# Kernel tuning notes

Hardware: AMD Instinct MI355X
Metric: run time of the kernel (lower is better)

Reference implementation:

```python
import jax, jax.numpy as jnp
import numpy as np

DROP_BLOCK = 7  # matches init_kwargs drop_block


def setup_inputs() -> dict:
    key = jax.random.key(0)
    k1, k2 = jax.random.split(key)
    x = jax.random.normal(k1, (32, 512, 56, 56), dtype=jnp.float32)
    T = jax.random.randint(k2, (32, 512, 1, 1), 0, 2, dtype=jnp.int32)
    return {"x": x, "T": T}


def _local_mask(x, T):
    B, C, H, W = x.shape
    xf = x.reshape(-1, H, W)                      # [B*C, H, W]
    marked = (T.reshape(-1) > 0)                  # [B*C] bool; which channels get a cutout
    # Argmax location per channel (original uses h for both div and mod)
    idx = jnp.argmax(xf.reshape(xf.shape[0], -1), axis=1)  # [B*C]
    mi = idx // H
    mj = idx % H
    half = DROP_BLOCK // 2  # floor(drop_block / 2)
    h1 = jnp.clip(mi - half, 0, H - 1)
    h2 = jnp.clip(mi + half, 0, H - 1)
    w1 = jnp.clip(mj - half, 0, W - 1)
    w2 = jnp.clip(mj + half, 0, W - 1)
    rows = jnp.arange(H)[None, :, None]           # [1, H, 1]
    cols = jnp.arange(W)[None, None, :]           # [1, 1, W]
    # S[i, h1:h2, w1:w2] = 0 (exclusive upper bound, as in torch slicing)
    in_box = ((rows >= h1[:, None, None]) & (rows < h2[:, None, None]) &
              (cols >= w1[:, None, None]) & (cols < w2[:, None, None]))
    S = jnp.where(in_box, 0.0, 1.0).astype(xf.dtype)       # [B*C, H, W]
    lam = (H * W) / S.sum(axis=(1, 2))                      # [B*C]
    masked = xf * S * lam[:, None, None]
    out = jnp.where(marked[:, None, None], masked, xf)
    return out.reshape(B, C, H, W)


def reference(x, T):
    return _local_mask(x, T)
```

## Files before the change

kernel.cpp:

```cpp
#include <hip/hip_runtime.h>

#define HH 56
#define WW 56
#define HW 3136
#define NV4 784
#define BLK 256

typedef float f4 __attribute__((ext_vector_type(4)));

__global__ __launch_bounds__(BLK, 8) void local_mask_kernel(
    const float* __restrict__ x, const int* __restrict__ T, float* __restrict__ out)
{
    const int ch  = blockIdx.x;
    const int tid = threadIdx.x;

    const bool marked = (T[ch] > 0);

    const f4* __restrict__ xin  = (const f4*)(x   + (size_t)ch * HW);
    f4* __restrict__       xout = (f4*)      (out + (size_t)ch * HW);

    f4 v[4];
    #pragma unroll
    for (int k = 0; k < 4; ++k) {
        int i = tid + k * BLK;
        if (i < NV4) v[k] = __builtin_nontemporal_load(&xin[i]);
    }

    if (!marked) {
        #pragma unroll
        for (int k = 0; k < 4; ++k) {
            int i = tid + k * BLK;
            if (i < NV4) __builtin_nontemporal_store(v[k], &xout[i]);
        }
        return;
    }

    float bestv = -__builtin_inff();
    int   besti = 0;
    #pragma unroll
    for (int k = 0; k < 4; ++k) {
        int i = tid + k * BLK;
        if (i < NV4) {
            const f4 f = v[k];
            const int base = i * 4;
            if (f.x > bestv) { bestv = f.x; besti = base;     }
            if (f.y > bestv) { bestv = f.y; besti = base + 1; }
            if (f.z > bestv) { bestv = f.z; besti = base + 2; }
            if (f.w > bestv) { bestv = f.w; besti = base + 3; }
        }
    }

    #pragma unroll
    for (int off = 32; off > 0; off >>= 1) {
        float ov = __shfl_down(bestv, (unsigned)off);
        int   oi = __shfl_down(besti, (unsigned)off);
        if (ov > bestv || (ov == bestv && oi < besti)) { bestv = ov; besti = oi; }
    }

    __shared__ float s_v[4];
    __shared__ int   s_i[4];

    const int wave = tid >> 6;
    const int lane = tid & 63;
    if (lane == 0) { s_v[wave] = bestv; s_i[wave] = besti; }
    __syncthreads();

    float bv = s_v[0]; int bi = s_i[0];
    #pragma unroll
    for (int w = 1; w < 4; ++w) {
        const float wv = s_v[w]; const int wi = s_i[w];
        if (wv > bv || (wv == bv && wi < bi)) { bv = wv; bi = wi; }
    }

    const int mi = bi / HH;
    const int mj = bi - mi * HH;
    const int h1 = max(mi - 3, 0);
    const int h2 = min(mi + 3, HH - 1);
    const int w1 = max(mj - 3, 0);
    const int w2 = min(mj + 3, WW - 1);
    const int zeros = (h2 - h1) * (w2 - w1);
    const float lam = (float)HW / (float)(HW - zeros);

    #pragma unroll
    for (int k = 0; k < 4; ++k) {
        int i = tid + k * BLK;
        if (i < NV4) {
            const f4  f    = v[k];
            const int row  = i / 14;
            const int col0 = (i - row * 14) * 4;
            const bool rin = (row >= h1) & (row < h2);
            f4 o;
            o.x = (rin & (col0     >= w1) & (col0     < w2)) ? 0.0f : f.x * lam;
            o.y = (rin & (col0 + 1 >= w1) & (col0 + 1 < w2)) ? 0.0f : f.y * lam;
            o.z = (rin & (col0 + 2 >= w1) & (col0 + 2 < w2)) ? 0.0f : f.z * lam;
            o.w = (rin & (col0 + 3 >= w1) & (col0 + 3 < w2)) ? 0.0f : f.w * lam;
            __builtin_nontemporal_store(o, &xout[i]);
        }
    }
}

extern "C" void kernel_launch(void* const* d_in, const int* in_sizes, int n_in,
                              void* d_out, int out_size, void* d_ws, size_t ws_size,
                              hipStream_t stream) {
    const float* x = (const float*)d_in[0];
    const int*   T = (const int*)d_in[1];
    float*     out = (float*)d_out;
    const int channels = in_sizes[0] / HW;
    local_mask_kernel<<<channels, BLK, 0, stream>>>(x, T, out);
}
```

Before: 324.1 us.

## Process multiple channels per block with double-buffered register prefetch

Each block now handles 8 channels in sequence. It loads the next channel's data into a second register buffer while computing and storing the current channel, with a single barrier per channel and double-buffered shared slots for the reduction. The aim is to hide load latency and amortize block launch overhead. In exchange, register pressure doubles, occupancy hints drop from 8 to 6 blocks, and the grid becomes 8x smaller, which could leave CUs underutilized.

```diff
diff --git a/kernel.cpp b/kernel.cpp
--- a/kernel.cpp
+++ b/kernel.cpp
@@ -5,97 +5,126 @@
 #define HW 3136
 #define NV4 784
 #define BLK 256
+#define CPB 8
 
 typedef float f4 __attribute__((ext_vector_type(4)));
 
-__global__ __launch_bounds__(BLK, 8) void local_mask_kernel(
-    const float* __restrict__ x, const int* __restrict__ T, float* __restrict__ out)
+__global__ __launch_bounds__(BLK, 6) void local_mask_kernel(
+    const float* __restrict__ x, const int* __restrict__ T, float* __restrict__ out,
+    int channels)
 {
-    const int ch  = blockIdx.x;
-    const int tid = threadIdx.x;
+    const int tid  = threadIdx.x;
+    const int wave = tid >> 6;
+    const int lane = tid & 63;
+    const int ch0  = blockIdx.x * CPB;
 
-    const bool marked = (T[ch] > 0);
+    __shared__ float s_v[2][4];
+    __shared__ int   s_i[2][4];
 
-    const f4* __restrict__ xin  = (const f4*)(x   + (size_t)ch * HW);
-    f4* __restrict__       xout = (f4*)      (out + (size_t)ch * HW);
-
-    f4 v[4];
+    int  idx[4], row4[4], c04[4];
+    bool act[4];
     #pragma unroll
     for (int k = 0; k < 4; ++k) {
-        int i = tid + k * BLK;
-        if (i < NV4) v[k] = __builtin_nontemporal_load(&xin[i]);
+        idx[k]  = tid + k * BLK;
+        act[k]  = idx[k] < NV4;
+        row4[k] = idx[k] / 14;
+        c04[k]  = (idx[k] - row4[k] * 14) * 4;
     }
 
-    if (!marked) {
+    f4 buf[2][4];
+
+    {
+        const f4* __restrict__ xin = (const f4*)(x + (size_t)ch0 * HW);
         #pragma unroll
-        for (int k = 0; k < 4; ++k) {
-            int i = tid + k * BLK;
-            if (i < NV4) __builtin_nontemporal_store(v[k], &xout[i]);
-        }
-        return;
+        for (int k = 0; k < 4; ++k)
+            if (act[k]) buf[0][k] = __builtin_nontemporal_load(&xin[idx[k]]);
     }
-
-    float bestv = -__builtin_inff();
-    int   besti = 0;
-    #pragma unroll
-    for (int k = 0; k < 4; ++k) {
-        int i = tid + k * BLK;
-        if (i < NV4) {
-            const f4 f = v[k];
-            const int base = i * 4;
-            if (f.x > bestv) { bestv = f.x; besti = base;     }
-            if (f.y > bestv) { bestv = f.y; besti = base + 1; }
-            if (f.z > bestv) { bestv = f.z; besti = base + 2; }
-            if (f.w > bestv) { bestv = f.w; besti = base + 3; }
-        }
-    }
+    int tcur = (ch0 < channels) ? T[ch0] : 0;
 
     #pragma unroll
-    for (int off = 32; off > 0; off >>= 1) {
-        float ov = __shfl_down(bestv, (unsigned)off);
-        int   oi = __shfl_down(besti, (unsigned)off);
-        if (ov > bestv || (ov == bestv && oi < besti)) { bestv = ov; besti = oi; }
-    }
+    for (int p = 0; p < CPB; ++p) {
+        const int cur = p & 1;
+        const int nxt = cur ^ 1;
+        const int c   = ch0 + p;
 
-    __shared__ float s_v[4];
-    __shared__ int   s_i[4];
+        int tnext = 0;
+        if ((p + 1 < CPB) & (c + 1 < channels)) {
+            tnext = T[c + 1];
+            const f4* __restrict__ xin = (const f4*)(x + (size_t)(c + 1) * HW);
+            #pragma unroll
+            for (int k = 0; k < 4; ++k)
+                if (act[k]) buf[nxt][k] = __builtin_nontemporal_load(&xin[idx[k]]);
+        }
 
-    const int wave = tid >> 6;
-    const int lane = tid & 63;
-    if (lane == 0) { s_v[wave] = bestv; s_i[wave] = besti; }
-    __syncthreads();
+        const bool inrange = (c < channels);
+        const bool marked  = inrange && (tcur > 0);
 
-    float bv = s_v[0]; int bi = s_i[0];
-    #pragma unroll
-    for (int w = 1; w < 4; ++w) {
-        const float wv = s_v[w]; const int wi = s_i[w];
-        if (wv > bv || (wv == bv && wi < bi)) { bv = wv; bi = wi; }
-    }
+        if (marked) {
+            float bestv = -__builtin_inff();
+            int   besti = 0;
+            #pragma unroll
+            for (int k = 0; k < 4; ++k) {
+                if (act[k]) {
+                    const f4  f    = buf[cur][k];
+                    const int base = idx[k] * 4;
+                    if (f.x > bestv) { bestv = f.x; besti = base;     }
+                    if (f.y > bestv) { bestv = f.y; besti = base + 1; }
+                    if (f.z > bestv) { bestv = f.z; besti = base + 2; }
+                    if (f.w > bestv) { bestv = f.w; besti = base + 3; }
+                }
+            }
+            #pragma unroll
+            for (int off = 32; off > 0; off >>= 1) {
+                float ov = __shfl_down(bestv, (unsigned)off);
+                int   oi = __shfl_down(besti, (unsigned)off);
+                if (ov > bestv || (ov == bestv && oi < besti)) { bestv = ov; besti = oi; }
+            }
+            if (lane == 0) { s_v[cur][wave] = bestv; s_i[cur][wave] = besti; }
+        }
 
-    const int mi = bi / HH;
-    const int mj = bi - mi * HH;
-    const int h1 = max(mi - 3, 0);
-    const int h2 = min(mi + 3, HH - 1);
-    const int w1 = max(mj - 3, 0);
-    const int w2 = min(mj + 3, WW - 1);
-    const int zeros = (h2 - h1) * (w2 - w1);
-    const float lam = (float)HW / (float)(HW - zeros);
+        asm volatile("s_waitcnt lgkmcnt(0)" ::: "memory");
+        __builtin_amdgcn_s_barrier();
+        asm volatile("" ::: "memory");
 
-    #pragma unroll
-    for (int k = 0; k < 4; ++k) {
-        int i = tid + k * BLK;
-        if (i < NV4) {
-            const f4  f    = v[k];
-            const int row  = i / 14;
-            const int col0 = (i - row * 14) * 4;
-            const bool rin = (row >= h1) & (row < h2);
-            f4 o;
-            o.x = (rin & (col0     >= w1) & (col0     < w2)) ? 0.0f : f.x * lam;
-            o.y = (rin & (col0 + 1 >= w1) & (col0 + 1 < w2)) ? 0.0f : f.y * lam;
-            o.z = (rin & (col0 + 2 >= w1) & (col0 + 2 < w2)) ? 0.0f : f.z * lam;
-            o.w = (rin & (col0 + 3 >= w1) & (col0 + 3 < w2)) ? 0.0f : f.w * lam;
-            __builtin_nontemporal_store(o, &xout[i]);
+        if (inrange) {
+            f4* __restrict__ xout = (f4*)(out + (size_t)c * HW);
+            if (marked) {
+                float bv = s_v[cur][0]; int bi = s_i[cur][0];
+                #pragma unroll
+                for (int w = 1; w < 4; ++w) {
+                    const float wv = s_v[cur][w]; const int wi = s_i[cur][w];
+                    if (wv > bv || (wv == bv && wi < bi)) { bv = wv; bi = wi; }
+                }
+                const int mi = bi / HH;
+                const int mj = bi - mi * HH;
+                const int h1 = max(mi - 3, 0);
+                const int h2 = min(mi + 3, HH - 1);
+                const int w1 = max(mj - 3, 0);
+                const int w2 = min(mj + 3, WW - 1);
+                const int zeros = (h2 - h1) * (w2 - w1);
+                const float lam = (float)HW / (float)(HW - zeros);
+
+                #pragma unroll
+                for (int k = 0; k < 4; ++k) {
+                    if (act[k]) {
+                        const f4   f   = buf[cur][k];
+                        const bool rin = (row4[k] >= h1) & (row4[k] < h2);
+                        const int  c0  = c04[k];
+                        f4 o;
+                        o.x = (rin & (c0     >= w1) & (c0     < w2)) ? 0.0f : f.x * lam;
+                        o.y = (rin & (c0 + 1 >= w1) & (c0 + 1 < w2)) ? 0.0f : f.y * lam;
+                        o.z = (rin & (c0 + 2 >= w1) & (c0 + 2 < w2)) ? 0.0f : f.z * lam;
+                        o.w = (rin & (c0 + 3 >= w1) & (c0 + 3 < w2)) ? 0.0f : f.w * lam;
+                        __builtin_nontemporal_store(o, &xout[idx[k]]);
+                    }
+                }
+            } else {
+                #pragma unroll
+                for (int k = 0; k < 4; ++k)
+                    if (act[k]) __builtin_nontemporal_store(buf[cur][k], &xout[idx[k]]);
+            }
         }
+        tcur = tnext;
     }
 }
 
@@ -106,5 +135,6 @@
     const int*   T = (const int*)d_in[1];
     float*     out = (float*)d_out;
     const int channels = in_sizes[0] / HW;
-    local_mask_kernel<<<channels, BLK, 0, stream>>>(x, T, out);
+    const int blocks   = (channels + CPB - 1) / CPB;
+    local_mask_kernel<<<blocks, BLK, 0, stream>>>(x, T, out, channels);
 }
```

Result: slower. 340.9 us (+5.2%).
